# Kernel tuning notes

Hardware: AMD Instinct MI355X
Metric: run time of the kernel (lower is better)

Reference implementation:

```python
import jax, jax.numpy as jnp
import numpy as np

B, S, H, F = 16, 2048, 1024, 1024


def sparsemax(z, axis):
    # standard sparsemax (Martins & Astudillo 2016) along `axis`
    z_sorted = -jnp.sort(-z, axis=axis)
    K = z.shape[axis]
    shp = [1] * z.ndim
    shp[axis] = K
    k = jnp.arange(1, K + 1, dtype=z.dtype).reshape(shp)
    cum = jnp.cumsum(z_sorted, axis=axis)
    support = (1.0 + k * z_sorted) > cum
    k_sel = jnp.sum(support, axis=axis, keepdims=True)
    cum_sel = jnp.take_along_axis(cum, k_sel.astype(jnp.int32) - 1, axis=axis)
    tau = (cum_sel - 1.0) / k_sel.astype(z.dtype)
    return jnp.maximum(z - tau, 0.0)


def additive_attention(query, values, w1, w2, attn_bias, v):
    # query: [B,F,1] -> permuted to [B,1,F]; values: [B,S,F]
    q = jnp.swapaxes(query, -2, -1)  # [B,1,F]
    t1 = q @ w1 + values @ w2        # [B,S,F] (broadcast over S)
    energy = jnp.tanh(t1 + attn_bias)
    return energy @ v                # [B,S,1]


def setup_inputs() -> dict:
    key = jax.random.key(0)
    ks = jax.random.split(key, 12)
    s = 0.02
    return {
        "attention_mask": jnp.ones((B, S), jnp.float32),
        "xlnet_output": jax.random.normal(ks[0], (B, S, H), jnp.float32),
        "item_weights": jax.random.uniform(ks[1], (B, S, 1), jnp.float32),
        "W_C": jax.random.normal(ks[2], (H, F), jnp.float32) * s,
        "b_C": jnp.zeros((F,), jnp.float32),
        "W_A": jax.random.normal(ks[3], (H, F), jnp.float32) * s,
        "b_A": jnp.zeros((F,), jnp.float32),
        "w1": jax.random.normal(ks[4], (F, F), jnp.float32) * s,
        "w2": jax.random.normal(ks[5], (F, F), jnp.float32) * s,
        "attn_bias": jnp.zeros((1, 1, F), jnp.float32),
        "v": jax.random.normal(ks[6], (F, 1), jnp.float32) * s,
        "w_1": jnp.ones((1,), jnp.float32),
        "w_2": jnp.ones((1,), jnp.float32),
        "w_3": jnp.ones((1,), jnp.float32),
        "layer_i": 0,
        "proactive_masking": 0,
    }


def reference(attention_mask, xlnet_output, item_weights, W_C, b_C, W_A, b_A,
              w1, w2, attn_bias, v, w_1, w_2, w_3, layer_i, proactive_masking):
    # attend-to-real-token mask: (1-m)*-10000 -> [B,S,1]
    mask_add = ((1.0 - attention_mask) * -10000.0)[..., None]
    # projections + ReLU (dropout in eval mode = identity; proactive_masking=0)
    C = jax.nn.relu(xlnet_output @ W_C + b_C)  # [B,S,F]
    A = jax.nn.relu(xlnet_output @ W_A + b_A)  # [B,S,F]
    # q = C^T @ item_weights -> [B,F,1]
    q = jnp.einsum('bsf,bso->bfo', C, item_weights)
    alpha = additive_attention(q, C, w1, w2, attn_bias, v) + mask_add
    alpha = jax.nn.softmax(alpha, axis=1)        # [B,S,1]
    h = jnp.einsum('bsf,bso->bfo', C, alpha)     # [B,F,1]
    L = additive_attention(h, A, w1, w2, attn_bias, v)  # [B,S,1]
    if layer_i == 0:
        x = w_3 ** 2 - w_2 ** 2 - w_1 ** 2
    elif layer_i == 1:
        x = w_3 ** 2 - w_2 ** 2
    else:
        x = w_3 ** 2
    L = L * jax.nn.sigmoid(x)
    L = L + mask_add
    L = sparsemax(L, axis=1)
    return (h, L, A)
```

## Files before the change

### kernel.cpp

```cpp
#include <hip/hip_runtime.h>
#include <hip/hip_bf16.h>
#include <math.h>

typedef __hip_bfloat16 bf16;
typedef __bf16 bf16x8 __attribute__((ext_vector_type(8)));
typedef float f32x4 __attribute__((ext_vector_type(4)));

#define BDIM 16
#define SDIM 2048
#define FDIM 1024
#define BS (BDIM * SDIM)

__device__ __forceinline__ float bf2f(bf16 x) { return __bfloat162float(x); }
__device__ __forceinline__ bf16 f2bf(float x) { return __float2bfloat16(x); }

template <int MODE, bool AF32, bool OUTF32>
__global__ __launch_bounds__(256) void gemm_bt(
    const void* __restrict__ Agv, const bf16* __restrict__ Bg,
    const float* __restrict__ bias, void* __restrict__ outp,
    const float* __restrict__ t1, const float* __restrict__ vvec,
    float* __restrict__ logit) {
  constexpr int BK = 32, K = 1024;
  __shared__ __align__(16) bf16 As[128 * BK];
  __shared__ __align__(16) bf16 Bs[128 * BK];

  const int tid = threadIdx.x;
  const int lane = tid & 63;
  const int wave = tid >> 6;
  const int wm = (wave & 1) * 64;
  const int wn = (wave >> 1) * 64;
  const int tile_m = blockIdx.x * 128;
  const int tile_n = blockIdx.y * 128;
  const int ln = lane & 15;
  const int ko = (lane >> 4) * 8;

  f32x4 acc[4][4] = {};

  const int arow = tid >> 2;
  const int acol = (tid & 3) * 8;
  const size_t aoff = (size_t)(tile_m + arow) * K + acol;
  const size_t aoff2 = aoff + (size_t)64 * K;
  const bf16* gB = Bg + (size_t)(tile_n + arow) * K + acol;
  const size_t rstep = (size_t)64 * K;
  bf16* lA = &As[arow * BK + acol];
  bf16* lA2 = &As[(64 + arow) * BK + acol];
  bf16* lB = &Bs[arow * BK + acol];
  bf16* lB2 = &Bs[(64 + arow) * BK + acol];

  for (int k0 = 0; k0 < K; k0 += BK) {
    bf16x8 va, va2;
    if constexpr (AF32) {
      const float* pa = (const float*)Agv + aoff + k0;
      const float* pa2 = (const float*)Agv + aoff2 + k0;
      const float4 x0 = *(const float4*)pa, x1 = *(const float4*)(pa + 4);
      const float4 y0 = *(const float4*)pa2, y1 = *(const float4*)(pa2 + 4);
      va[0] = (__bf16)x0.x; va[1] = (__bf16)x0.y; va[2] = (__bf16)x0.z; va[3] = (__bf16)x0.w;
      va[4] = (__bf16)x1.x; va[5] = (__bf16)x1.y; va[6] = (__bf16)x1.z; va[7] = (__bf16)x1.w;
      va2[0] = (__bf16)y0.x; va2[1] = (__bf16)y0.y; va2[2] = (__bf16)y0.z; va2[3] = (__bf16)y0.w;
      va2[4] = (__bf16)y1.x; va2[5] = (__bf16)y1.y; va2[6] = (__bf16)y1.z; va2[7] = (__bf16)y1.w;
    } else {
      va = *(const bf16x8*)((const bf16*)Agv + aoff + k0);
      va2 = *(const bf16x8*)((const bf16*)Agv + aoff2 + k0);
    }
    const bf16x8 vb = *(const bf16x8*)(gB + k0);
    const bf16x8 vb2 = *(const bf16x8*)(gB + k0 + rstep);
    __syncthreads();
    *(bf16x8*)lA = va;
    *(bf16x8*)lA2 = va2;
    *(bf16x8*)lB = vb;
    *(bf16x8*)lB2 = vb2;
    __syncthreads();
    bf16x8 af[4], bfr[4];
#pragma unroll
    for (int i = 0; i < 4; i++)
      af[i] = *(const bf16x8*)&As[(wm + i * 16 + ln) * BK + ko];
#pragma unroll
    for (int j = 0; j < 4; j++)
      bfr[j] = *(const bf16x8*)&Bs[(wn + j * 16 + ln) * BK + ko];
#pragma unroll
    for (int i = 0; i < 4; i++)
#pragma unroll
      for (int j = 0; j < 4; j++)
        acc[i][j] =
            __builtin_amdgcn_mfma_f32_16x16x32_bf16(af[i], bfr[j], acc[i][j], 0, 0, 0);
  }

  if (MODE == 0) {
#pragma unroll
    for (int i = 0; i < 4; i++) {
#pragma unroll
      for (int j = 0; j < 4; j++) {
        const int colg = tile_n + wn + j * 16 + ln;
        const float bv = bias[colg];
#pragma unroll
        for (int r = 0; r < 4; r++) {
          const int rowg = tile_m + wm + i * 16 + ((lane >> 4) << 2) + r;
          const float val = fmaxf(acc[i][j][r] + bv, 0.f);
          if constexpr (OUTF32)
            ((float*)outp)[(size_t)rowg * FDIM + colg] = val;
          else
            ((bf16*)outp)[(size_t)rowg * FDIM + colg] = f2bf(val);
        }
      }
    }
  } else {
    const int b = tile_m >> 11;
    float tcol[4], vcol[4];
#pragma unroll
    for (int j = 0; j < 4; j++) {
      const int colg = tile_n + wn + j * 16 + ln;
      tcol[j] = t1[b * FDIM + colg];
      vcol[j] = vvec[colg];
    }
#pragma unroll
    for (int i = 0; i < 4; i++) {
#pragma unroll
      for (int r = 0; r < 4; r++) {
        float s = 0.f;
#pragma unroll
        for (int j = 0; j < 4; j++) s += tanhf(acc[i][j][r] + tcol[j]) * vcol[j];
        s += __shfl_xor(s, 1);
        s += __shfl_xor(s, 2);
        s += __shfl_xor(s, 4);
        s += __shfl_xor(s, 8);
        if (ln == 0) {
          const int rowg = tile_m + wm + i * 16 + ((lane >> 4) << 2) + r;
          atomicAdd(&logit[rowg], s);
        }
      }
    }
  }
}

__global__ void transpose_cvt_k(const float* __restrict__ src, bf16* __restrict__ dst,
                                int K, int N) {
  __shared__ bf16 t[32][33];
  const int n0 = blockIdx.x * 32, k0 = blockIdx.y * 32;
  const int tx = threadIdx.x, ty = threadIdx.y;
  for (int i = 0; i < 32; i += 8)
    t[ty + i][tx] = f2bf(src[(size_t)(k0 + ty + i) * N + n0 + tx]);
  __syncthreads();
  for (int i = 0; i < 32; i += 8)
    dst[(size_t)(n0 + ty + i) * K + k0 + tx] = t[tx][ty + i];
}

__global__ void zerof_k(float* __restrict__ a, int n) {
  const int i = blockIdx.x * 256 + threadIdx.x;
  if (i < n) a[i] = 0.f;
}

__global__ void copyf_k(const float* __restrict__ in, float* __restrict__ out, int n) {
  const int i = blockIdx.x * 256 + threadIdx.x;
  if (i < n) out[i] = in[i];
}

__global__ void colreduce_k(const bf16* __restrict__ M, const float* __restrict__ w,
                            float* __restrict__ outf) {
  const int b = blockIdx.y;
  const int f = blockIdx.x * 256 + threadIdx.x;
  const int s0 = blockIdx.z * 128;
  const bf16* col = M + ((size_t)b * SDIM + s0) * FDIM + f;
  const float* wb = w + b * SDIM + s0;
  float acc = 0.f;
#pragma unroll 8
  for (int s = 0; s < 128; ++s) acc += bf2f(col[(size_t)s * FDIM]) * wb[s];
  atomicAdd(&outf[b * FDIM + f], acc);
}

__global__ void smallgemm_k(const float* __restrict__ invec, const float* __restrict__ w1,
                            const float* __restrict__ bias, float* __restrict__ out) {
  const int b = blockIdx.y;
  const int n = blockIdx.x * 256 + threadIdx.x;
  const float* q = invec + b * FDIM;
  float acc = 0.f;
#pragma unroll 8
  for (int f = 0; f < FDIM; ++f) acc += q[f] * w1[(size_t)f * FDIM + n];
  out[b * FDIM + n] = acc + bias[n];
}

__global__ void softmax_k(const float* __restrict__ logit, const float* __restrict__ mask,
                          float* __restrict__ alpha) {
  const int b = blockIdx.x, tid = threadIdx.x;
  __shared__ float red[4];
  float v[8];
  float lmax = -1e30f;
#pragma unroll
  for (int k = 0; k < 8; ++k) {
    const int s = tid + k * 256;
    const float m = (1.f - mask[b * SDIM + s]) * -10000.f;
    v[k] = logit[b * SDIM + s] + m;
    lmax = fmaxf(lmax, v[k]);
  }
  for (int m = 1; m < 64; m <<= 1) lmax = fmaxf(lmax, __shfl_xor(lmax, m));
  if ((tid & 63) == 0) red[tid >> 6] = lmax;
  __syncthreads();
  lmax = fmaxf(fmaxf(red[0], red[1]), fmaxf(red[2], red[3]));
  __syncthreads();
  float lsum = 0.f;
#pragma unroll
  for (int k = 0; k < 8; ++k) {
    v[k] = expf(v[k] - lmax);
    lsum += v[k];
  }
  for (int m = 1; m < 64; m <<= 1) lsum += __shfl_xor(lsum, m);
  if ((tid & 63) == 0) red[tid >> 6] = lsum;
  __syncthreads();
  const float inv = 1.f / (red[0] + red[1] + red[2] + red[3]);
#pragma unroll
  for (int k = 0; k < 8; ++k) alpha[b * SDIM + tid + k * 256] = v[k] * inv;
}

__global__ void sparsemax_k(const float* __restrict__ Ll, const float* __restrict__ mask,
                            const float* __restrict__ w1s, const float* __restrict__ w2s,
                            const float* __restrict__ w3s, const int* __restrict__ layer_i,
                            float* __restrict__ Lout) {
  const int b = blockIdx.x, tid = threadIdx.x;
  __shared__ float red[4];
  const float a1 = w1s[0], a2 = w2s[0], a3 = w3s[0];
  const int li = layer_i[0];
  const float x = (li == 0) ? (a3 * a3 - a2 * a2 - a1 * a1)
                            : ((li == 1) ? (a3 * a3 - a2 * a2) : (a3 * a3));
  const float sig = 1.f / (1.f + expf(-x));
  float z[8];
  float lmax = -1e30f;
#pragma unroll
  for (int k = 0; k < 8; ++k) {
    const int s = tid + k * 256;
    const float m = (1.f - mask[b * SDIM + s]) * -10000.f;
    z[k] = Ll[b * SDIM + s] * sig + m;
    lmax = fmaxf(lmax, z[k]);
  }
  for (int m = 1; m < 64; m <<= 1) lmax = fmaxf(lmax, __shfl_xor(lmax, m));
  if ((tid & 63) == 0) red[tid >> 6] = lmax;
  __syncthreads();
  const float zmax = fmaxf(fmaxf(red[0], red[1]), fmaxf(red[2], red[3]));
  __syncthreads();
  float lo = zmax - 1.f, hi = zmax;
  for (int it = 0; it < 40; ++it) {
    const float tau = 0.5f * (lo + hi);
    float ssum = 0.f;
#pragma unroll
    for (int k = 0; k < 8; ++k) ssum += fmaxf(z[k] - tau, 0.f);
    for (int m = 1; m < 64; m <<= 1) ssum += __shfl_xor(ssum, m);
    if ((tid & 63) == 0) red[tid >> 6] = ssum;
    __syncthreads();
    const float tot = red[0] + red[1] + red[2] + red[3];
    __syncthreads();
    if (tot > 1.f) lo = tau; else hi = tau;
  }
  const float tau = 0.5f * (lo + hi);
#pragma unroll
  for (int k = 0; k < 8; ++k)
    Lout[b * SDIM + tid + k * 256] = fmaxf(z[k] - tau, 0.f);
}

extern "C" void kernel_launch(void* const* d_in, const int* in_sizes, int n_in,
                              void* d_out, int out_size, void* d_ws, size_t ws_size,
                              hipStream_t stream) {
  const float* mask = (const float*)d_in[0];
  const float* xlnet = (const float*)d_in[1];
  const float* iw = (const float*)d_in[2];
  const float* W_C = (const float*)d_in[3];
  const float* b_C = (const float*)d_in[4];
  const float* W_A = (const float*)d_in[5];
  const float* b_A = (const float*)d_in[6];
  const float* w1 = (const float*)d_in[7];
  const float* w2 = (const float*)d_in[8];
  const float* attn_bias = (const float*)d_in[9];
  const float* v = (const float*)d_in[10];
  const float* w_1 = (const float*)d_in[11];
  const float* w_2 = (const float*)d_in[12];
  const float* w_3 = (const float*)d_in[13];
  const int* layer_i = (const int*)d_in[14];

  float* out = (float*)d_out;
  float* h_out = out;
  float* L_out = out + 16384;
  float* A_out = out + 49152;
  bf16* Cbuf = (bf16*)A_out;

  char* ws = (char*)d_ws;
  bf16* WT_C = (bf16*)(ws);
  bf16* WT_A = (bf16*)(ws + 2097152);
  bf16* w2T = (bf16*)(ws + 4194304);
  float* qbuf = (float*)(ws + 6291456);
  float* t1q = (float*)(ws + 6356992);
  float* t1h = (float*)(ws + 6422528);
  float* hbuf = (float*)(ws + 6488064);
  float* a_logit = (float*)(ws + 6553600);
  float* alpha = (float*)(ws + 6684672);
  float* L_logit = (float*)(ws + 6815744);

  const dim3 tb(32, 8);
  transpose_cvt_k<<<dim3(32, 32), tb, 0, stream>>>(W_C, WT_C, 1024, 1024);
  transpose_cvt_k<<<dim3(32, 32), tb, 0, stream>>>(W_A, WT_A, 1024, 1024);
  transpose_cvt_k<<<dim3(32, 32), tb, 0, stream>>>(w2, w2T, 1024, 1024);
  zerof_k<<<640, 256, 0, stream>>>(qbuf, 163840);

  gemm_bt<0, true, false><<<dim3(BS / 128, 8), 256, 0, stream>>>(
      xlnet, WT_C, b_C, Cbuf, nullptr, nullptr, nullptr);
  colreduce_k<<<dim3(4, BDIM, 16), 256, 0, stream>>>(Cbuf, iw, qbuf);
  smallgemm_k<<<dim3(4, BDIM), 256, 0, stream>>>(qbuf, w1, attn_bias, t1q);
  gemm_bt<1, false, false><<<dim3(BS / 128, 8), 256, 0, stream>>>(
      Cbuf, w2T, nullptr, nullptr, t1q, v, a_logit);
  softmax_k<<<BDIM, 256, 0, stream>>>(a_logit, mask, alpha);
  colreduce_k<<<dim3(4, BDIM, 16), 256, 0, stream>>>(Cbuf, alpha, hbuf);
  copyf_k<<<64, 256, 0, stream>>>(hbuf, h_out, BDIM * FDIM);
  smallgemm_k<<<dim3(4, BDIM), 256, 0, stream>>>(hbuf, w1, attn_bias, t1h);
  gemm_bt<0, true, true><<<dim3(BS / 128, 8), 256, 0, stream>>>(
      xlnet, WT_A, b_A, A_out, nullptr, nullptr, nullptr);
  gemm_bt<1, true, false><<<dim3(BS / 128, 8), 256, 0, stream>>>(
      A_out, w2T, nullptr, nullptr, t1h, v, L_logit);
  sparsemax_k<<<BDIM, 256, 0, stream>>>(L_logit, mask, w_1, w_2, w_3, layer_i, L_out);
}
```

Before: 900.3 us.

## Use direct global-to-LDS loads with pre-converted bf16 inputs for GEMMs

Adds a new GEMM kernel that loads A and B tiles straight into LDS with global_load_lds, which needs bf16 operands. To feed it, xlnet_output is converted to bf16 once and reused by both projection GEMMs, and the A projection also writes a bf16 copy for the following energy GEMM. The fallback kernel gets padded LDS rows to reduce bank conflicts. This trades extra workspace and an extra conversion pass for cheaper loads inside the GEMMs, and the new path runs only when the workspace is large enough.

After: 828.5 us. 8.0% less time.

```diff
diff --git a/kernel.cpp b/kernel.cpp
--- a/kernel.cpp
+++ b/kernel.cpp
@@ -14,12 +14,18 @@
 __device__ __forceinline__ float bf2f(bf16 x) { return __bfloat162float(x); }
 __device__ __forceinline__ bf16 f2bf(float x) { return __float2bfloat16(x); }
 
-template <int MODE, bool AF32, bool OUTF32>
-__global__ __launch_bounds__(256) void gemm_bt(
-    const void* __restrict__ Agv, const bf16* __restrict__ Bg,
-    const float* __restrict__ bias, void* __restrict__ outp,
-    const float* __restrict__ t1, const float* __restrict__ vvec,
-    float* __restrict__ logit) {
+__device__ __forceinline__ void gload16(const void* g, void* l) {
+  __builtin_amdgcn_global_load_lds(
+      (const __attribute__((address_space(1))) unsigned int*)g,
+      (__attribute__((address_space(3))) unsigned int*)l, 16, 0, 0);
+}
+
+template <int MODE, int OUTK>
+__global__ __launch_bounds__(256) void gemm_glds(
+    const bf16* __restrict__ Ag, const bf16* __restrict__ Bg,
+    const float* __restrict__ bias, bf16* __restrict__ outb,
+    float* __restrict__ outf, const float* __restrict__ t1,
+    const float* __restrict__ vvec, float* __restrict__ logit) {
   constexpr int BK = 32, K = 1024;
   __shared__ __align__(16) bf16 As[128 * BK];
   __shared__ __align__(16) bf16 Bs[128 * BK];
@@ -36,16 +42,117 @@
 
   f32x4 acc[4][4] = {};
 
+  const int lrow = wave * 16 + (lane >> 2);
+  const int lcolb = (lane & 3) * 16;
+  const char* gA0 = (const char*)(Ag + (size_t)(tile_m + lrow) * K) + lcolb;
+  const char* gA1 = (const char*)(Ag + (size_t)(tile_m + lrow + 64) * K) + lcolb;
+  const char* gB0 = (const char*)(Bg + (size_t)(tile_n + lrow) * K) + lcolb;
+  const char* gB1 = (const char*)(Bg + (size_t)(tile_n + lrow + 64) * K) + lcolb;
+  char* lA0 = (char*)As + wave * 1024;
+  char* lA1 = lA0 + 4096;
+  char* lB0 = (char*)Bs + wave * 1024;
+  char* lB1 = lB0 + 4096;
+
+  for (int k0 = 0; k0 < K; k0 += BK) {
+    __syncthreads();
+    gload16(gA0, lA0);
+    gload16(gA1, lA1);
+    gload16(gB0, lB0);
+    gload16(gB1, lB1);
+    gA0 += 64; gA1 += 64; gB0 += 64; gB1 += 64;
+    __syncthreads();
+    bf16x8 af[4], bfr[4];
+#pragma unroll
+    for (int i = 0; i < 4; i++)
+      af[i] = *(const bf16x8*)&As[(wm + i * 16 + ln) * BK + ko];
+#pragma unroll
+    for (int j = 0; j < 4; j++)
+      bfr[j] = *(const bf16x8*)&Bs[(wn + j * 16 + ln) * BK + ko];
+#pragma unroll
+    for (int i = 0; i < 4; i++)
+#pragma unroll
+      for (int j = 0; j < 4; j++)
+        acc[i][j] =
+            __builtin_amdgcn_mfma_f32_16x16x32_bf16(af[i], bfr[j], acc[i][j], 0, 0, 0);
+  }
+
+  if (MODE == 0) {
+#pragma unroll
+    for (int i = 0; i < 4; i++) {
+#pragma unroll
+      for (int j = 0; j < 4; j++) {
+        const int colg = tile_n + wn + j * 16 + ln;
+        const float bv = bias[colg];
+#pragma unroll
+        for (int r = 0; r < 4; r++) {
+          const int rowg = tile_m + wm + i * 16 + ((lane >> 4) << 2) + r;
+          const float val = fmaxf(acc[i][j][r] + bv, 0.f);
+          if constexpr (OUTK != 1) outb[(size_t)rowg * FDIM + colg] = f2bf(val);
+          if constexpr (OUTK != 0) outf[(size_t)rowg * FDIM + colg] = val;
+        }
+      }
+    }
+  } else {
+    const int b = tile_m >> 11;
+    float tcol[4], vcol[4];
+#pragma unroll
+    for (int j = 0; j < 4; j++) {
+      const int colg = tile_n + wn + j * 16 + ln;
+      tcol[j] = t1[b * FDIM + colg];
+      vcol[j] = vvec[colg];
+    }
+#pragma unroll
+    for (int i = 0; i < 4; i++) {
+#pragma unroll
+      for (int r = 0; r < 4; r++) {
+        float s = 0.f;
+#pragma unroll
+        for (int j = 0; j < 4; j++) s += tanhf(acc[i][j][r] + tcol[j]) * vcol[j];
+        s += __shfl_xor(s, 1);
+        s += __shfl_xor(s, 2);
+        s += __shfl_xor(s, 4);
+        s += __shfl_xor(s, 8);
+        if (ln == 0) {
+          const int rowg = tile_m + wm + i * 16 + ((lane >> 4) << 2) + r;
+          atomicAdd(&logit[rowg], s);
+        }
+      }
+    }
+  }
+}
+
+template <int MODE, bool AF32, bool OUTF32>
+__global__ __launch_bounds__(256) void gemm_bt(
+    const void* __restrict__ Agv, const bf16* __restrict__ Bg,
+    const float* __restrict__ bias, void* __restrict__ outp,
+    const float* __restrict__ t1, const float* __restrict__ vvec,
+    float* __restrict__ logit) {
+  constexpr int BK = 32, K = 1024, LDP = 56;
+  __shared__ __align__(16) bf16 As[128 * LDP];
+  __shared__ __align__(16) bf16 Bs[128 * LDP];
+
+  const int tid = threadIdx.x;
+  const int lane = tid & 63;
+  const int wave = tid >> 6;
+  const int wm = (wave & 1) * 64;
+  const int wn = (wave >> 1) * 64;
+  const int tile_m = blockIdx.x * 128;
+  const int tile_n = blockIdx.y * 128;
+  const int ln = lane & 15;
+  const int ko = (lane >> 4) * 8;
+
+  f32x4 acc[4][4] = {};
+
   const int arow = tid >> 2;
   const int acol = (tid & 3) * 8;
   const size_t aoff = (size_t)(tile_m + arow) * K + acol;
   const size_t aoff2 = aoff + (size_t)64 * K;
   const bf16* gB = Bg + (size_t)(tile_n + arow) * K + acol;
   const size_t rstep = (size_t)64 * K;
-  bf16* lA = &As[arow * BK + acol];
-  bf16* lA2 = &As[(64 + arow) * BK + acol];
-  bf16* lB = &Bs[arow * BK + acol];
-  bf16* lB2 = &Bs[(64 + arow) * BK + acol];
+  bf16* lA = &As[arow * LDP + acol];
+  bf16* lA2 = &As[(64 + arow) * LDP + acol];
+  bf16* lB = &Bs[arow * LDP + acol];
+  bf16* lB2 = &Bs[(64 + arow) * LDP + acol];
 
   for (int k0 = 0; k0 < K; k0 += BK) {
     bf16x8 va, va2;
@@ -73,10 +180,10 @@
     bf16x8 af[4], bfr[4];
 #pragma unroll
     for (int i = 0; i < 4; i++)
-      af[i] = *(const bf16x8*)&As[(wm + i * 16 + ln) * BK + ko];
+      af[i] = *(const bf16x8*)&As[(wm + i * 16 + ln) * LDP + ko];
 #pragma unroll
     for (int j = 0; j < 4; j++)
-      bfr[j] = *(const bf16x8*)&Bs[(wn + j * 16 + ln) * BK + ko];
+      bfr[j] = *(const bf16x8*)&Bs[(wn + j * 16 + ln) * LDP + ko];
 #pragma unroll
     for (int i = 0; i < 4; i++)
 #pragma unroll
@@ -142,6 +249,16 @@
   __syncthreads();
   for (int i = 0; i < 32; i += 8)
     dst[(size_t)(n0 + ty + i) * K + k0 + tx] = t[tx][ty + i];
+}
+
+__global__ void cvt_bf16_k(const float* __restrict__ in, bf16* __restrict__ out) {
+  const size_t i = ((size_t)blockIdx.x * 256 + threadIdx.x) * 8;
+  const float4 a = *(const float4*)(in + i);
+  const float4 b = *(const float4*)(in + i + 4);
+  bf16x8 o;
+  o[0] = (__bf16)a.x; o[1] = (__bf16)a.y; o[2] = (__bf16)a.z; o[3] = (__bf16)a.w;
+  o[4] = (__bf16)b.x; o[5] = (__bf16)b.y; o[6] = (__bf16)b.z; o[7] = (__bf16)b.w;
+  *(bf16x8*)(out + i) = o;
 }
 
 __global__ void zerof_k(float* __restrict__ a, int n) {
@@ -290,6 +407,10 @@
   float* a_logit = (float*)(ws + 6553600);
   float* alpha = (float*)(ws + 6684672);
   float* L_logit = (float*)(ws + 6815744);
+  bf16* Xbf = (bf16*)(ws + 6946816);
+  bf16* Abf = (bf16*)(ws + 74055680);
+  const bool t1ok = ws_size >= (size_t)74055680;
+  const bool t2ok = ws_size >= (size_t)141164544;
 
   const dim3 tb(32, 8);
   transpose_cvt_k<<<dim3(32, 32), tb, 0, stream>>>(W_C, WT_C, 1024, 1024);
@@ -297,19 +418,44 @@
   transpose_cvt_k<<<dim3(32, 32), tb, 0, stream>>>(w2, w2T, 1024, 1024);
   zerof_k<<<640, 256, 0, stream>>>(qbuf, 163840);
 
-  gemm_bt<0, true, false><<<dim3(BS / 128, 8), 256, 0, stream>>>(
-      xlnet, WT_C, b_C, Cbuf, nullptr, nullptr, nullptr);
+  const dim3 gg(BS / 128, FDIM / 128);
+
+  if (t1ok)
+    cvt_bf16_k<<<16384, 256, 0, stream>>>(xlnet, Xbf);
+
+  if (t1ok)
+    gemm_glds<0, 0><<<gg, 256, 0, stream>>>(Xbf, WT_C, b_C, Cbuf, nullptr,
+                                            nullptr, nullptr, nullptr);
+  else
+    gemm_bt<0, true, false><<<gg, 256, 0, stream>>>(xlnet, WT_C, b_C, Cbuf,
+                                                    nullptr, nullptr, nullptr);
   colreduce_k<<<dim3(4, BDIM, 16), 256, 0, stream>>>(Cbuf, iw, qbuf);
   smallgemm_k<<<dim3(4, BDIM), 256, 0, stream>>>(qbuf, w1, attn_bias, t1q);
-  gemm_bt<1, false, false><<<dim3(BS / 128, 8), 256, 0, stream>>>(
-      Cbuf, w2T, nullptr, nullptr, t1q, v, a_logit);
+  if (t1ok)
+    gemm_glds<1, 0><<<gg, 256, 0, stream>>>(Cbuf, w2T, nullptr, nullptr,
+                                            nullptr, t1q, v, a_logit);
+  else
+    gemm_bt<1, false, false><<<gg, 256, 0, stream>>>(Cbuf, w2T, nullptr,
+                                                     nullptr, t1q, v, a_logit);
   softmax_k<<<BDIM, 256, 0, stream>>>(a_logit, mask, alpha);
   colreduce_k<<<dim3(4, BDIM, 16), 256, 0, stream>>>(Cbuf, alpha, hbuf);
   copyf_k<<<64, 256, 0, stream>>>(hbuf, h_out, BDIM * FDIM);
   smallgemm_k<<<dim3(4, BDIM), 256, 0, stream>>>(hbuf, w1, attn_bias, t1h);
-  gemm_bt<0, true, true><<<dim3(BS / 128, 8), 256, 0, stream>>>(
-      xlnet, WT_A, b_A, A_out, nullptr, nullptr, nullptr);
-  gemm_bt<1, true, false><<<dim3(BS / 128, 8), 256, 0, stream>>>(
-      A_out, w2T, nullptr, nullptr, t1h, v, L_logit);
+
+  if (t2ok)
+    gemm_glds<0, 2><<<gg, 256, 0, stream>>>(Xbf, WT_A, b_A, Abf, A_out,
+                                            nullptr, nullptr, nullptr);
+  else if (t1ok)
+    gemm_glds<0, 1><<<gg, 256, 0, stream>>>(Xbf, WT_A, b_A, nullptr, A_out,
+                                            nullptr, nullptr, nullptr);
+  else
+    gemm_bt<0, true, true><<<gg, 256, 0, stream>>>(xlnet, WT_A, b_A, A_out,
+                                                   nullptr, nullptr, nullptr);
+  if (t2ok)
+    gemm_glds<1, 0><<<gg, 256, 0, stream>>>(Abf, w2T, nullptr, nullptr,
+                                            nullptr, t1h, v, L_logit);
+  else
+    gemm_bt<1, true, false><<<gg, 256, 0, stream>>>(A_out, w2T, nullptr,
+                                                    nullptr, t1h, v, L_logit);
   sparsemax_k<<<BDIM, 256, 0, stream>>>(L_logit, mask, w_1, w_2, w_3, layer_i, L_out);
 }
```
